# Kernel optimization log

Measured on AMD Instinct MI355X. Metric: run time of the kernel, lower is better.

The kernel has to match this reference:

```python
import jax, jax.numpy as jnp
import numpy as np

B, L, H, E, R = 4, 512, 768, 10, 10

def setup_inputs() -> dict:
    key = jax.random.key(0)
    ks = jax.random.split(key, 7)
    s = 1.0 / np.sqrt(H)
    return {
        "h": jax.random.normal(ks[0], (B, L, H), dtype=jnp.float32),
        "W_proj": jax.random.normal(ks[1], (H, H), dtype=jnp.float32) * s,
        "b_proj": jax.random.normal(ks[2], (H,), dtype=jnp.float32) * s,
        "W_ent": jax.random.normal(ks[3], (E, H), dtype=jnp.float32) * s,
        "b_ent": jax.random.normal(ks[4], (E,), dtype=jnp.float32) * s,
        "W_bil": jax.random.normal(ks[5], (R, H, H), dtype=jnp.float32) * s,
        "b_bil": jax.random.normal(ks[6], (R,), dtype=jnp.float32) * s,
    }

def reference(h, W_proj, b_proj, W_ent, b_ent, W_bil, b_bil):
    # h: (B, L, H)
    h_proj = jax.nn.relu(jnp.einsum('blh,kh->blk', h, W_proj) + b_proj)  # Linear: x @ W^T + b
    ent_logits = jnp.einsum('blh,eh->ble', h_proj, W_ent) + b_ent        # (B, L, E)
    # nn.Bilinear on all (i, j) pairs: rel[b,i,j,r] = h_i^T W_r h_j + b_r.
    # Factored O(L^2*H*R + L*H^2*R) instead of materializing (B,L,L,H) pairs.
    t = jnp.einsum('rhk,bmk->brmh', W_bil, h_proj)                        # (B, R, L, H)
    rel_logits = jnp.einsum('blh,brmh->blmr', h_proj, t) + b_bil          # (B, L, L, R)
    return (ent_logits, rel_logits)
```

## Files before the change

kernel.cpp:

```cpp
#include <hip/hip_runtime.h>
#include <stdint.h>

#define Bdim 4
#define Ldim 512
#define Hdim 768
#define Edim 10
#define Rdim 10

typedef __attribute__((ext_vector_type(8))) short short8;
typedef __attribute__((ext_vector_type(4))) float floatx4;

__device__ __forceinline__ unsigned short f2bf(float x) {
    unsigned int u = __float_as_uint(x);
    unsigned int r = (u + 0x7fffu + ((u >> 16) & 1u)) >> 16;
    return (unsigned short)r;
}
__device__ __forceinline__ float bf2f(unsigned short u) {
    return __uint_as_float(((unsigned int)u) << 16);
}

#define GLOAD_LDS16(g, l)                                                      \
    __builtin_amdgcn_global_load_lds(                                          \
        (const __attribute__((address_space(1))) void*)(g),                    \
        (__attribute__((address_space(3))) void*)(l), 16, 0, 0)

#define WAITVM(n) asm volatile("s_waitcnt vmcnt(" #n ")" ::: "memory")

__device__ __forceinline__ int xcd_swz(int bid, int nwg) {
    int cpx = nwg >> 3;
    return (bid & 7) * cpx + (bid >> 3);
}

__device__ __forceinline__ void gemm_bt_core256_cnt(
    const unsigned short* __restrict__ A, int lda,
    const unsigned short* __restrict__ Bm, int ldb,
    unsigned short* lA, unsigned short* lB,
    floatx4 acc[8][4])
{
    const int tid  = threadIdx.x;
    const int lane = tid & 63;
    const int wave = tid >> 6;
    const int wr = wave >> 2;
    const int wc = wave & 3;

    const int srow   = tid >> 3;
    const int schunk = (tid & 7) ^ (srow & 7);
    const int skk    = schunk << 3;

    const int frow = lane & 15;
    const int fs   = lane >> 4;

    #define STAGE256(t, buf)                                                   \
        do {                                                                   \
            const int k0s = (t) << 6;                                          \
            unsigned short* dA = lA + (buf) * 16384;                           \
            unsigned short* dB = lB + (buf) * 16384;                           \
            _Pragma("unroll")                                                  \
            for (int i = 0; i < 4; ++i) {                                      \
                GLOAD_LDS16(A  + (size_t)(srow + 64 * i) * lda + k0s + skk,    \
                            dA + (tid + 512 * i) * 8);                         \
                GLOAD_LDS16(Bm + (size_t)(srow + 64 * i) * ldb + k0s + skk,    \
                            dB + (tid + 512 * i) * 8);                         \
            }                                                                  \
        } while (0)

    #define COMPUTE256(buf)                                                    \
        do {                                                                   \
            const unsigned short* sA = lA + (buf) * 16384;                     \
            const unsigned short* sB = lB + (buf) * 16384;                     \
            _Pragma("unroll")                                                  \
            for (int h = 0; h < 2; ++h) {                                      \
                short8 bfr[4];                                                 \
                _Pragma("unroll")                                              \
                for (int ni = 0; ni < 4; ++ni) {                               \
                    int row  = wc * 64 + ni * 16 + frow;                       \
                    int slot = (fs + 4 * h) ^ (row & 7);                       \
                    bfr[ni] = *reinterpret_cast<const short8*>(                \
                        sB + row * 64 + slot * 8);                             \
                }                                                              \
                _Pragma("unroll")                                              \
                for (int mi = 0; mi < 8; ++mi) {                               \
                    int row  = wr * 128 + mi * 16 + frow;                      \
                    int slot = (fs + 4 * h) ^ (row & 7);                       \
                    short8 af = *reinterpret_cast<const short8*>(              \
                        sA + row * 64 + slot * 8);                             \
                    _Pragma("unroll")                                          \
                    for (int ni = 0; ni < 4; ++ni)                             \
                        acc[mi][ni] = __builtin_amdgcn_mfma_f32_16x16x32_bf16( \
                            af, bfr[ni], acc[mi][ni], 0, 0, 0);                \
                }                                                              \
            }                                                                  \
        } while (0)

    const int NT = Hdim >> 6;

    STAGE256(0, 0);
    for (int kt = 0; kt < NT - 1; ++kt) {
        __builtin_amdgcn_s_barrier();
        STAGE256(kt + 1, (kt + 1) & 1);
        WAITVM(8);
        __builtin_amdgcn_s_barrier();
        __builtin_amdgcn_sched_barrier(0);
        COMPUTE256(kt & 1);
    }
    __builtin_amdgcn_s_barrier();
    WAITVM(0);
    __builtin_amdgcn_s_barrier();
    __builtin_amdgcn_sched_barrier(0);
    COMPUTE256((NT - 1) & 1);

    #undef STAGE256
    #undef COMPUTE256
}

__global__ __launch_bounds__(256) void k_prep(
    const float* __restrict__ h,   const float* __restrict__ Wp,
    const float* __restrict__ bproj,
    const float* __restrict__ Wbil, const float* __restrict__ We,
    unsigned short* __restrict__ hp,
    unsigned short* __restrict__ Wb_bf, unsigned short* __restrict__ We_bf)
{
    __shared__ unsigned short lA[128 * 64];
    __shared__ unsigned short lB[128 * 64];
    const int tid = threadIdx.x;

    if (blockIdx.x >= 96) {
        const int n2 = Rdim * Hdim * Hdim / 4;
        const int n3 = Edim * Hdim / 4;
        int i = (blockIdx.x - 96) * 256 + tid;
        const int stride = (gridDim.x - 96) * 256;
        for (; i < n2 + n3; i += stride) {
            const float* s; unsigned short* d; int j = i;
            if (j < n2) { s = Wbil; d = Wb_bf; }
            else { j -= n2; s = We; d = We_bf; }
            float4 v = reinterpret_cast<const float4*>(s)[j];
            ushort4 o;
            o.x = f2bf(v.x); o.y = f2bf(v.y); o.z = f2bf(v.z); o.w = f2bf(v.w);
            reinterpret_cast<ushort4*>(d)[j] = o;
        }
        return;
    }

    int bid = xcd_swz(blockIdx.x, 96);
    const int m0 = (bid % 16) * 128;
    const int n0 = (bid / 16) * 128;
    const float* Asrc = h  + (size_t)m0 * Hdim;
    const float* Bsrc = Wp + (size_t)n0 * Hdim;

    const int lane = tid & 63;
    const int wave = tid >> 6;
    const int wr = wave >> 1, wc = wave & 1;
    const int frow = lane & 15;
    const int fs   = lane >> 4;

    floatx4 acc[4][4];
    #pragma unroll
    for (int i = 0; i < 4; ++i)
        #pragma unroll
        for (int j = 0; j < 4; ++j)
            acc[i][j] = (floatx4){0.f, 0.f, 0.f, 0.f};

    float4 ra[4][2], rb[4][2];
    #define LOADREGS(k0s)                                                      \
        _Pragma("unroll")                                                      \
        for (int i = 0; i < 4; ++i) {                                          \
            int q = tid + 256 * i, row = q >> 3, pchk = q & 7;                 \
            int lchk = pchk ^ (row & 7);                                       \
            const float* sa = Asrc + (size_t)row * Hdim + (k0s) + lchk * 8;    \
            const float* sb = Bsrc + (size_t)row * Hdim + (k0s) + lchk * 8;    \
            ra[i][0] = *reinterpret_cast<const float4*>(sa);                   \
            ra[i][1] = *reinterpret_cast<const float4*>(sa + 4);               \
            rb[i][0] = *reinterpret_cast<const float4*>(sb);                   \
            rb[i][1] = *reinterpret_cast<const float4*>(sb + 4);               \
        }

    LOADREGS(0);
    const int NT = Hdim >> 6;
    for (int kt = 0; kt < NT; ++kt) {
        short8 pa[4], pb[4];
        #pragma unroll
        for (int i = 0; i < 4; ++i) {
            pa[i][0] = f2bf(ra[i][0].x); pa[i][1] = f2bf(ra[i][0].y);
            pa[i][2] = f2bf(ra[i][0].z); pa[i][3] = f2bf(ra[i][0].w);
            pa[i][4] = f2bf(ra[i][1].x); pa[i][5] = f2bf(ra[i][1].y);
            pa[i][6] = f2bf(ra[i][1].z); pa[i][7] = f2bf(ra[i][1].w);
            pb[i][0] = f2bf(rb[i][0].x); pb[i][1] = f2bf(rb[i][0].y);
            pb[i][2] = f2bf(rb[i][0].z); pb[i][3] = f2bf(rb[i][0].w);
            pb[i][4] = f2bf(rb[i][1].x); pb[i][5] = f2bf(rb[i][1].y);
            pb[i][6] = f2bf(rb[i][1].z); pb[i][7] = f2bf(rb[i][1].w);
        }
        __syncthreads();
        #pragma unroll
        for (int i = 0; i < 4; ++i) {
            int q = tid + 256 * i, row = q >> 3, pchk = q & 7;
            *reinterpret_cast<short8*>(lA + row * 64 + pchk * 8) = pa[i];
            *reinterpret_cast<short8*>(lB + row * 64 + pchk * 8) = pb[i];
        }
        if (kt + 1 < NT) LOADREGS((kt + 1) << 6);
        __syncthreads();
        #pragma unroll
        for (int hh = 0; hh < 2; ++hh) {
            short8 af[4], bfr[4];
            #pragma unroll
            for (int mi = 0; mi < 4; ++mi) {
                int row  = wr * 64 + mi * 16 + frow;
                int slot = (fs + 4 * hh) ^ (row & 7);
                af[mi] = *reinterpret_cast<const short8*>(lA + row * 64 + slot * 8);
            }
            #pragma unroll
            for (int ni = 0; ni < 4; ++ni) {
                int row  = wc * 64 + ni * 16 + frow;
                int slot = (fs + 4 * hh) ^ (row & 7);
                bfr[ni] = *reinterpret_cast<const short8*>(lB + row * 64 + slot * 8);
            }
            #pragma unroll
            for (int mi = 0; mi < 4; ++mi)
                #pragma unroll
                for (int ni = 0; ni < 4; ++ni)
                    acc[mi][ni] = __builtin_amdgcn_mfma_f32_16x16x32_bf16(
                        af[mi], bfr[ni], acc[mi][ni], 0, 0, 0);
        }
    }
    #undef LOADREGS

    const int cl = lane & 15, rh = (lane >> 4) * 4;
    #pragma unroll
    for (int mi = 0; mi < 4; ++mi)
        #pragma unroll
        for (int ni = 0; ni < 4; ++ni)
            #pragma unroll
            for (int j = 0; j < 4; ++j) {
                int r = m0 + wr * 64 + mi * 16 + rh + j;
                int c = n0 + wc * 64 + ni * 16 + cl;
                float v = acc[mi][ni][j] + bproj[c];
                hp[(size_t)r * Hdim + c] = f2bf(fmaxf(v, 0.0f));
            }
}

__global__ __launch_bounds__(512, 1) void k_gemm_t(
    const unsigned short* __restrict__ hp,
    const unsigned short* __restrict__ Wb,
    unsigned short* __restrict__ T)
{
    __shared__ unsigned short lA[2 * 256 * 64];
    __shared__ unsigned short lB[2 * 256 * 64];
    int bid = xcd_swz(blockIdx.x + gridDim.x * blockIdx.y, gridDim.x * gridDim.y);
    const int m0 = (bid % gridDim.x) * 256;
    const int n0 = (bid / gridDim.x) * 256;
    floatx4 acc[8][4];
    #pragma unroll
    for (int i = 0; i < 8; ++i)
        #pragma unroll
        for (int j = 0; j < 4; ++j)
            acc[i][j] = (floatx4){0.f, 0.f, 0.f, 0.f};

    gemm_bt_core256_cnt(hp + (size_t)m0 * Hdim, Hdim,
                        Wb + (size_t)n0 * Hdim, Hdim, lA, lB, acc);

    const int tid = threadIdx.x, lane = tid & 63, wave = tid >> 6;
    const int wr = wave >> 2, wc = wave & 3;
    const int cl = lane & 15, rh = (lane >> 4) * 4;
    #pragma unroll
    for (int mi = 0; mi < 8; ++mi)
        #pragma unroll
        for (int ni = 0; ni < 4; ++ni)
            #pragma unroll
            for (int j = 0; j < 4; ++j) {
                int r = m0 + wr * 128 + mi * 16 + rh + j;
                int c = n0 + wc * 64 + ni * 16 + cl;
                T[(size_t)r * (Rdim * Hdim) + c] = f2bf(acc[mi][ni][j]);
            }
}

__global__ __launch_bounds__(512, 1) void k_rel_ent(
    const unsigned short* __restrict__ hp,
    const unsigned short* __restrict__ T,
    const float* __restrict__ bbil,
    float* __restrict__ rel,
    const unsigned short* __restrict__ We,
    const float* __restrict__ bent,
    float* __restrict__ out_ent)
{
    __shared__ unsigned short lA[2 * 256 * 64];
    __shared__ unsigned short lB[2 * 256 * 64];
    const int tid = threadIdx.x, lane = tid & 63, wave = tid >> 6;

    if (blockIdx.x >= 160) {
        const int e = blockIdx.x - 160;
        const int base = (e * 8 + wave) * 8;
        for (int rr = 0; rr < 8; ++rr) {
            const unsigned short* row = hp + (size_t)(base + rr) * Hdim;
            float hv[12];
            #pragma unroll
            for (int j = 0; j < 12; ++j) hv[j] = bf2f(row[lane + j * 64]);
            #pragma unroll
            for (int ee = 0; ee < Edim; ++ee) {
                const unsigned short* wrow = We + ee * Hdim;
                float s = 0.f;
                #pragma unroll
                for (int j = 0; j < 12; ++j) s += hv[j] * bf2f(wrow[lane + j * 64]);
                #pragma unroll
                for (int off = 32; off >= 1; off >>= 1) s += __shfl_xor(s, off);
                if (lane == 0) out_ent[(size_t)(base + rr) * Edim + ee] = s + bent[ee];
            }
        }
        return;
    }

    int bid = xcd_swz(blockIdx.x, 160);
    const int m0 = (bid & 7) * 256;
    const int n0 = (bid >> 3) * 256;
    const int b  = m0 >> 9;
    floatx4 acc[8][4];
    #pragma unroll
    for (int i = 0; i < 8; ++i)
        #pragma unroll
        for (int j = 0; j < 4; ++j)
            acc[i][j] = (floatx4){0.f, 0.f, 0.f, 0.f};

    const unsigned short* Ab = hp + (size_t)m0 * Hdim;
    const unsigned short* Bb = T + (size_t)b * Ldim * (Rdim * Hdim) + (size_t)n0 * Hdim;
    gemm_bt_core256_cnt(Ab, Hdim, Bb, Hdim, lA, lB, acc);

    const int wr = wave >> 2, wc = wave & 3;
    const int cl = lane & 15, rh = (lane >> 4) * 4;
    #pragma unroll
    for (int mi = 0; mi < 8; ++mi)
        #pragma unroll
        for (int ni = 0; ni < 4; ++ni) {
            int n = n0 + wc * 64 + ni * 16 + cl;
            float bias = bbil[n % Rdim];
            #pragma unroll
            for (int j = 0; j < 4; ++j) {
                int grow = m0 + wr * 128 + mi * 16 + rh + j;
                rel[(size_t)grow * (Ldim * Rdim) + n] = acc[mi][ni][j] + bias;
            }
        }
}

extern "C" void kernel_launch(void* const* d_in, const int* in_sizes, int n_in,
                              void* d_out, int out_size, void* d_ws, size_t ws_size,
                              hipStream_t stream)
{
    const float* h     = (const float*)d_in[0];
    const float* Wproj = (const float*)d_in[1];
    const float* bproj = (const float*)d_in[2];
    const float* Went  = (const float*)d_in[3];
    const float* bent  = (const float*)d_in[4];
    const float* Wbil  = (const float*)d_in[5];
    const float* bbil  = (const float*)d_in[6];

    float* out_ent = (float*)d_out;
    float* out_rel = (float*)d_out + (size_t)Bdim * Ldim * Edim;

    unsigned short* Wb_bf = (unsigned short*)d_ws;
    unsigned short* We_bf = Wb_bf + (size_t)Rdim * Hdim * Hdim;
    unsigned short* hp_bf = We_bf + (size_t)Edim * Hdim;
    unsigned short* T_bf  = hp_bf + (size_t)2048 * Hdim;

    k_prep<<<dim3(1120), 256, 0, stream>>>(h, Wproj, bproj, Wbil, Went,
                                           hp_bf, Wb_bf, We_bf);

    k_gemm_t<<<dim3(2048 / 256, (Rdim * Hdim) / 256), 512, 0, stream>>>(hp_bf, Wb_bf, T_bf);

    k_rel_ent<<<dim3(192), 512, 0, stream>>>(hp_bf, T_bf, bbil, out_rel,
                                             We_bf, bent, out_ent);
}
```

Before: 169.4 us.

## Retile relation GEMM to 256x160 tiles and move entity head into T-GEMM launch

The entity-logit blocks move from the relation kernel into the T-projection GEMM launch, which now runs 240 GEMM tiles plus 32 entity blocks in one grid. The relation GEMM gets its own kernel with 256x160 output tiles, giving 256 blocks instead of 160 so all CUs are covered. It has a custom double-buffered LDS pipeline and a 4x2 wave layout where each wave computes 64x80. This trades the tuned 256x256 core for a narrower tile with lower per-block reuse and more hand-written loading code, in exchange for better load balance across the GPU.

```diff
diff --git a/kernel.cpp b/kernel.cpp
--- a/kernel.cpp
+++ b/kernel.cpp
@@ -237,46 +237,10 @@
             }
 }
 
-__global__ __launch_bounds__(512, 1) void k_gemm_t(
+__global__ __launch_bounds__(512, 1) void k_gemm_t_ent(
     const unsigned short* __restrict__ hp,
     const unsigned short* __restrict__ Wb,
-    unsigned short* __restrict__ T)
-{
-    __shared__ unsigned short lA[2 * 256 * 64];
-    __shared__ unsigned short lB[2 * 256 * 64];
-    int bid = xcd_swz(blockIdx.x + gridDim.x * blockIdx.y, gridDim.x * gridDim.y);
-    const int m0 = (bid % gridDim.x) * 256;
-    const int n0 = (bid / gridDim.x) * 256;
-    floatx4 acc[8][4];
-    #pragma unroll
-    for (int i = 0; i < 8; ++i)
-        #pragma unroll
-        for (int j = 0; j < 4; ++j)
-            acc[i][j] = (floatx4){0.f, 0.f, 0.f, 0.f};
-
-    gemm_bt_core256_cnt(hp + (size_t)m0 * Hdim, Hdim,
-                        Wb + (size_t)n0 * Hdim, Hdim, lA, lB, acc);
-
-    const int tid = threadIdx.x, lane = tid & 63, wave = tid >> 6;
-    const int wr = wave >> 2, wc = wave & 3;
-    const int cl = lane & 15, rh = (lane >> 4) * 4;
-    #pragma unroll
-    for (int mi = 0; mi < 8; ++mi)
-        #pragma unroll
-        for (int ni = 0; ni < 4; ++ni)
-            #pragma unroll
-            for (int j = 0; j < 4; ++j) {
-                int r = m0 + wr * 128 + mi * 16 + rh + j;
-                int c = n0 + wc * 64 + ni * 16 + cl;
-                T[(size_t)r * (Rdim * Hdim) + c] = f2bf(acc[mi][ni][j]);
-            }
-}
-
-__global__ __launch_bounds__(512, 1) void k_rel_ent(
-    const unsigned short* __restrict__ hp,
-    const unsigned short* __restrict__ T,
-    const float* __restrict__ bbil,
-    float* __restrict__ rel,
+    unsigned short* __restrict__ T,
     const unsigned short* __restrict__ We,
     const float* __restrict__ bent,
     float* __restrict__ out_ent)
@@ -285,9 +249,8 @@
     __shared__ unsigned short lB[2 * 256 * 64];
     const int tid = threadIdx.x, lane = tid & 63, wave = tid >> 6;
 
-    if (blockIdx.x >= 160) {
-        const int e = blockIdx.x - 160;
-        const int base = (e * 8 + wave) * 8;
+    if (blockIdx.x >= 240) {
+        const int base = ((blockIdx.x - 240) * 8 + wave) * 8;
         for (int rr = 0; rr < 8; ++rr) {
             const unsigned short* row = hp + (size_t)(base + rr) * Hdim;
             float hv[12];
@@ -307,10 +270,9 @@
         return;
     }
 
-    int bid = xcd_swz(blockIdx.x, 160);
-    const int m0 = (bid & 7) * 256;
-    const int n0 = (bid >> 3) * 256;
-    const int b  = m0 >> 9;
+    int bid = xcd_swz(blockIdx.x, 240);
+    const int m0 = (bid % 8) * 256;
+    const int n0 = (bid / 8) * 256;
     floatx4 acc[8][4];
     #pragma unroll
     for (int i = 0; i < 8; ++i)
@@ -318,21 +280,131 @@
         for (int j = 0; j < 4; ++j)
             acc[i][j] = (floatx4){0.f, 0.f, 0.f, 0.f};
 
-    const unsigned short* Ab = hp + (size_t)m0 * Hdim;
-    const unsigned short* Bb = T + (size_t)b * Ldim * (Rdim * Hdim) + (size_t)n0 * Hdim;
-    gemm_bt_core256_cnt(Ab, Hdim, Bb, Hdim, lA, lB, acc);
+    gemm_bt_core256_cnt(hp + (size_t)m0 * Hdim, Hdim,
+                        Wb + (size_t)n0 * Hdim, Hdim, lA, lB, acc);
 
     const int wr = wave >> 2, wc = wave & 3;
     const int cl = lane & 15, rh = (lane >> 4) * 4;
     #pragma unroll
     for (int mi = 0; mi < 8; ++mi)
         #pragma unroll
-        for (int ni = 0; ni < 4; ++ni) {
-            int n = n0 + wc * 64 + ni * 16 + cl;
+        for (int ni = 0; ni < 4; ++ni)
+            #pragma unroll
+            for (int j = 0; j < 4; ++j) {
+                int r = m0 + wr * 128 + mi * 16 + rh + j;
+                int c = n0 + wc * 64 + ni * 16 + cl;
+                T[(size_t)r * (Rdim * Hdim) + c] = f2bf(acc[mi][ni][j]);
+            }
+}
+
+__global__ __launch_bounds__(512, 1) void k_rel(
+    const unsigned short* __restrict__ hp,
+    const unsigned short* __restrict__ T,
+    const float* __restrict__ bbil,
+    float* __restrict__ rel)
+{
+    __shared__ unsigned short lA[2 * 256 * 64];
+    __shared__ unsigned short lB[2 * 192 * 64];
+    const int tid = threadIdx.x, lane = tid & 63, wave = tid >> 6;
+    const int wr = wave >> 1;
+    const int wv = wave & 1;
+
+    int bid = xcd_swz(blockIdx.x, 256);
+    const int m0 = (bid & 7) * 256;
+    const int n0 = (bid >> 3) * 160;
+    const int b  = m0 >> 9;
+
+    const unsigned short* A  = hp + (size_t)m0 * Hdim;
+    const unsigned short* Bm = T + (size_t)b * Ldim * (Rdim * Hdim) + (size_t)n0 * Hdim;
+
+    const int srow   = tid >> 3;
+    const int schunk = (tid & 7) ^ (srow & 7);
+    const int skk    = schunk << 3;
+    const int brow2  = (srow >= 32) ? (srow + 64) : (srow + 128);
+
+    const int frow = lane & 15;
+    const int fs   = lane >> 4;
+
+    floatx4 acc[4][5];
+    #pragma unroll
+    for (int i = 0; i < 4; ++i)
+        #pragma unroll
+        for (int j = 0; j < 5; ++j)
+            acc[i][j] = (floatx4){0.f, 0.f, 0.f, 0.f};
+
+    #define STAGE_R(t, buf)                                                    \
+        do {                                                                   \
+            const int k0s = (t) << 6;                                          \
+            unsigned short* dA = lA + (buf) * 16384;                           \
+            unsigned short* dB = lB + (buf) * 12288;                           \
+            _Pragma("unroll")                                                  \
+            for (int i = 0; i < 4; ++i)                                        \
+                GLOAD_LDS16(A + (size_t)(srow + 64 * i) * Hdim + k0s + skk,    \
+                            dA + (tid + 512 * i) * 8);                         \
+            GLOAD_LDS16(Bm + (size_t)srow * Hdim + k0s + skk,                  \
+                        dB + tid * 8);                                         \
+            GLOAD_LDS16(Bm + (size_t)(srow + 64) * Hdim + k0s + skk,           \
+                        dB + (tid + 512) * 8);                                 \
+            GLOAD_LDS16(Bm + (size_t)brow2 * Hdim + k0s + skk,                 \
+                        dB + (tid + 1024) * 8);                                \
+        } while (0)
+
+    #define COMPUTE_R(buf)                                                     \
+        do {                                                                   \
+            const unsigned short* sA = lA + (buf) * 16384;                     \
+            const unsigned short* sB = lB + (buf) * 12288;                     \
+            _Pragma("unroll")                                                  \
+            for (int h = 0; h < 2; ++h) {                                      \
+                short8 bfr[5];                                                 \
+                _Pragma("unroll")                                              \
+                for (int ni = 0; ni < 5; ++ni) {                               \
+                    int row  = wv * 80 + ni * 16 + frow;                       \
+                    int slot = (fs + 4 * h) ^ (row & 7);                       \
+                    bfr[ni] = *reinterpret_cast<const short8*>(                \
+                        sB + row * 64 + slot * 8);                             \
+                }                                                              \
+                _Pragma("unroll")                                              \
+                for (int mi = 0; mi < 4; ++mi) {                               \
+                    int row  = wr * 64 + mi * 16 + frow;                       \
+                    int slot = (fs + 4 * h) ^ (row & 7);                       \
+                    short8 af = *reinterpret_cast<const short8*>(              \
+                        sA + row * 64 + slot * 8);                             \
+                    _Pragma("unroll")                                          \
+                    for (int ni = 0; ni < 5; ++ni)                             \
+                        acc[mi][ni] = __builtin_amdgcn_mfma_f32_16x16x32_bf16( \
+                            af, bfr[ni], acc[mi][ni], 0, 0, 0);                \
+                }                                                              \
+            }                                                                  \
+        } while (0)
+
+    const int NT = Hdim >> 6;
+    STAGE_R(0, 0);
+    for (int kt = 0; kt < NT - 1; ++kt) {
+        __builtin_amdgcn_s_barrier();
+        STAGE_R(kt + 1, (kt + 1) & 1);
+        WAITVM(7);
+        __builtin_amdgcn_s_barrier();
+        __builtin_amdgcn_sched_barrier(0);
+        COMPUTE_R(kt & 1);
+    }
+    __builtin_amdgcn_s_barrier();
+    WAITVM(0);
+    __builtin_amdgcn_s_barrier();
+    __builtin_amdgcn_sched_barrier(0);
+    COMPUTE_R((NT - 1) & 1);
+    #undef STAGE_R
+    #undef COMPUTE_R
+
+    const int cl = lane & 15, rh = (lane >> 4) * 4;
+    #pragma unroll
+    for (int mi = 0; mi < 4; ++mi)
+        #pragma unroll
+        for (int ni = 0; ni < 5; ++ni) {
+            int n = n0 + wv * 80 + ni * 16 + cl;
             float bias = bbil[n % Rdim];
             #pragma unroll
             for (int j = 0; j < 4; ++j) {
-                int grow = m0 + wr * 128 + mi * 16 + rh + j;
+                int grow = m0 + wr * 64 + mi * 16 + rh + j;
                 rel[(size_t)grow * (Ldim * Rdim) + n] = acc[mi][ni][j] + bias;
             }
         }
@@ -361,8 +433,8 @@
     k_prep<<<dim3(1120), 256, 0, stream>>>(h, Wproj, bproj, Wbil, Went,
                                            hp_bf, Wb_bf, We_bf);
 
-    k_gemm_t<<<dim3(2048 / 256, (Rdim * Hdim) / 256), 512, 0, stream>>>(hp_bf, Wb_bf, T_bf);
-
-    k_rel_ent<<<dim3(192), 512, 0, stream>>>(hp_bf, T_bf, bbil, out_rel,
-                                             We_bf, bent, out_ent);
-}
+    k_gemm_t_ent<<<dim3(272), 512, 0, stream>>>(hp_bf, Wb_bf, T_bf,
+                                                We_bf, bent, out_ent);
+
+    k_rel<<<dim3(256), 512, 0, stream>>>(hp_bf, T_bf, bbil, out_rel);
+}
```

After: 187.0 us. 1.1x slower.

## Switch GEMMs to 128x128 single-buffered tiles and move entity head into T kernel

Applied to the files above, without the earlier changes.

Replaces the 256x256, 512-thread double-buffered GEMM core with a 128x128, 256-thread single-buffered core running several blocks per CU. The smaller tiles produce more workgroups (960 for T, 640 for rel) to fill the CUs better, and occupancy replaces the explicit prefetch pipeline as the latency hiding. The entity-logit computation moves from the rel kernel into the T-GEMM kernel. The trade-off is lower per-tile data reuse and no explicit overlap of loads with MFMA.

```diff
diff --git a/kernel.cpp b/kernel.cpp
--- a/kernel.cpp
+++ b/kernel.cpp
@@ -24,93 +24,60 @@
         (const __attribute__((address_space(1))) void*)(g),                    \
         (__attribute__((address_space(3))) void*)(l), 16, 0, 0)
 
-#define WAITVM(n) asm volatile("s_waitcnt vmcnt(" #n ")" ::: "memory")
-
 __device__ __forceinline__ int xcd_swz(int bid, int nwg) {
     int cpx = nwg >> 3;
     return (bid & 7) * cpx + (bid >> 3);
 }
 
-__device__ __forceinline__ void gemm_bt_core256_cnt(
+__device__ __forceinline__ void gemm_bt_core128_sb(
     const unsigned short* __restrict__ A, int lda,
     const unsigned short* __restrict__ Bm, int ldb,
     unsigned short* lA, unsigned short* lB,
-    floatx4 acc[8][4])
+    floatx4 acc[4][4])
 {
     const int tid  = threadIdx.x;
     const int lane = tid & 63;
     const int wave = tid >> 6;
-    const int wr = wave >> 2;
-    const int wc = wave & 3;
-
-    const int srow   = tid >> 3;
-    const int schunk = (tid & 7) ^ (srow & 7);
-    const int skk    = schunk << 3;
-
+    const int wr = wave >> 1;
+    const int wc = wave & 1;
     const int frow = lane & 15;
     const int fs   = lane >> 4;
 
-    #define STAGE256(t, buf)                                                   \
-        do {                                                                   \
-            const int k0s = (t) << 6;                                          \
-            unsigned short* dA = lA + (buf) * 16384;                           \
-            unsigned short* dB = lB + (buf) * 16384;                           \
-            _Pragma("unroll")                                                  \
-            for (int i = 0; i < 4; ++i) {                                      \
-                GLOAD_LDS16(A  + (size_t)(srow + 64 * i) * lda + k0s + skk,    \
-                            dA + (tid + 512 * i) * 8);                         \
-                GLOAD_LDS16(Bm + (size_t)(srow + 64 * i) * ldb + k0s + skk,    \
-                            dB + (tid + 512 * i) * 8);                         \
-            }                                                                  \
-        } while (0)
-
-    #define COMPUTE256(buf)                                                    \
-        do {                                                                   \
-            const unsigned short* sA = lA + (buf) * 16384;                     \
-            const unsigned short* sB = lB + (buf) * 16384;                     \
-            _Pragma("unroll")                                                  \
-            for (int h = 0; h < 2; ++h) {                                      \
-                short8 bfr[4];                                                 \
-                _Pragma("unroll")                                              \
-                for (int ni = 0; ni < 4; ++ni) {                               \
-                    int row  = wc * 64 + ni * 16 + frow;                       \
-                    int slot = (fs + 4 * h) ^ (row & 7);                       \
-                    bfr[ni] = *reinterpret_cast<const short8*>(                \
-                        sB + row * 64 + slot * 8);                             \
-                }                                                              \
-                _Pragma("unroll")                                              \
-                for (int mi = 0; mi < 8; ++mi) {                               \
-                    int row  = wr * 128 + mi * 16 + frow;                      \
-                    int slot = (fs + 4 * h) ^ (row & 7);                       \
-                    short8 af = *reinterpret_cast<const short8*>(              \
-                        sA + row * 64 + slot * 8);                             \
-                    _Pragma("unroll")                                          \
-                    for (int ni = 0; ni < 4; ++ni)                             \
-                        acc[mi][ni] = __builtin_amdgcn_mfma_f32_16x16x32_bf16( \
-                            af, bfr[ni], acc[mi][ni], 0, 0, 0);                \
-                }                                                              \
-            }                                                                  \
-        } while (0)
-
     const int NT = Hdim >> 6;
-
-    STAGE256(0, 0);
-    for (int kt = 0; kt < NT - 1; ++kt) {
-        __builtin_amdgcn_s_barrier();
-        STAGE256(kt + 1, (kt + 1) & 1);
-        WAITVM(8);
-        __builtin_amdgcn_s_barrier();
-        __builtin_amdgcn_sched_barrier(0);
-        COMPUTE256(kt & 1);
+    for (int kt = 0; kt < NT; ++kt) {
+        const int k0 = kt << 6;
+        if (kt) __builtin_amdgcn_s_barrier();
+        #pragma unroll
+        for (int i = 0; i < 4; ++i) {
+            int q = tid + 256 * i, row = q >> 3, pchk = q & 7;
+            int lchk = pchk ^ (row & 7);
+            GLOAD_LDS16(A  + (size_t)row * lda + k0 + lchk * 8, lA + q * 8);
+            GLOAD_LDS16(Bm + (size_t)row * ldb + k0 + lchk * 8, lB + q * 8);
+        }
+        __syncthreads();
+        #pragma unroll
+        for (int h = 0; h < 2; ++h) {
+            short8 af[4], bfr[4];
+            #pragma unroll
+            for (int mi = 0; mi < 4; ++mi) {
+                int row  = wr * 64 + mi * 16 + frow;
+                int slot = (fs + 4 * h) ^ (row & 7);
+                af[mi] = *reinterpret_cast<const short8*>(lA + row * 64 + slot * 8);
+            }
+            #pragma unroll
+            for (int ni = 0; ni < 4; ++ni) {
+                int row  = wc * 64 + ni * 16 + frow;
+                int slot = (fs + 4 * h) ^ (row & 7);
+                bfr[ni] = *reinterpret_cast<const short8*>(lB + row * 64 + slot * 8);
+            }
+            #pragma unroll
+            for (int mi = 0; mi < 4; ++mi)
+                #pragma unroll
+                for (int ni = 0; ni < 4; ++ni)
+                    acc[mi][ni] = __builtin_amdgcn_mfma_f32_16x16x32_bf16(
+                        af[mi], bfr[ni], acc[mi][ni], 0, 0, 0);
+        }
     }
-    __builtin_amdgcn_s_barrier();
-    WAITVM(0);
-    __builtin_amdgcn_s_barrier();
-    __builtin_amdgcn_sched_barrier(0);
-    COMPUTE256((NT - 1) & 1);
-
-    #undef STAGE256
-    #undef COMPUTE256
 }
 
 __global__ __launch_bounds__(256) void k_prep(
@@ -237,58 +204,21 @@
             }
 }
 
-__global__ __launch_bounds__(512, 1) void k_gemm_t(
+__global__ __launch_bounds__(256, 4) void k_gemm_t_ent(
     const unsigned short* __restrict__ hp,
     const unsigned short* __restrict__ Wb,
-    unsigned short* __restrict__ T)
-{
-    __shared__ unsigned short lA[2 * 256 * 64];
-    __shared__ unsigned short lB[2 * 256 * 64];
-    int bid = xcd_swz(blockIdx.x + gridDim.x * blockIdx.y, gridDim.x * gridDim.y);
-    const int m0 = (bid % gridDim.x) * 256;
-    const int n0 = (bid / gridDim.x) * 256;
-    floatx4 acc[8][4];
-    #pragma unroll
-    for (int i = 0; i < 8; ++i)
-        #pragma unroll
-        for (int j = 0; j < 4; ++j)
-            acc[i][j] = (floatx4){0.f, 0.f, 0.f, 0.f};
-
-    gemm_bt_core256_cnt(hp + (size_t)m0 * Hdim, Hdim,
-                        Wb + (size_t)n0 * Hdim, Hdim, lA, lB, acc);
-
-    const int tid = threadIdx.x, lane = tid & 63, wave = tid >> 6;
-    const int wr = wave >> 2, wc = wave & 3;
-    const int cl = lane & 15, rh = (lane >> 4) * 4;
-    #pragma unroll
-    for (int mi = 0; mi < 8; ++mi)
-        #pragma unroll
-        for (int ni = 0; ni < 4; ++ni)
-            #pragma unroll
-            for (int j = 0; j < 4; ++j) {
-                int r = m0 + wr * 128 + mi * 16 + rh + j;
-                int c = n0 + wc * 64 + ni * 16 + cl;
-                T[(size_t)r * (Rdim * Hdim) + c] = f2bf(acc[mi][ni][j]);
-            }
-}
-
-__global__ __launch_bounds__(512, 1) void k_rel_ent(
-    const unsigned short* __restrict__ hp,
-    const unsigned short* __restrict__ T,
-    const float* __restrict__ bbil,
-    float* __restrict__ rel,
+    unsigned short* __restrict__ T,
     const unsigned short* __restrict__ We,
     const float* __restrict__ bent,
     float* __restrict__ out_ent)
 {
-    __shared__ unsigned short lA[2 * 256 * 64];
-    __shared__ unsigned short lB[2 * 256 * 64];
+    __shared__ unsigned short lA[128 * 64];
+    __shared__ unsigned short lB[128 * 64];
     const int tid = threadIdx.x, lane = tid & 63, wave = tid >> 6;
 
-    if (blockIdx.x >= 160) {
-        const int e = blockIdx.x - 160;
-        const int base = (e * 8 + wave) * 8;
-        for (int rr = 0; rr < 8; ++rr) {
+    if (blockIdx.x < 16) {
+        const int base = (blockIdx.x * 4 + wave) * 32;
+        for (int rr = 0; rr < 32; ++rr) {
             const unsigned short* row = hp + (size_t)(base + rr) * Hdim;
             float hv[12];
             #pragma unroll
@@ -307,32 +237,69 @@
         return;
     }
 
-    int bid = xcd_swz(blockIdx.x, 160);
-    const int m0 = (bid & 7) * 256;
-    const int n0 = (bid >> 3) * 256;
-    const int b  = m0 >> 9;
-    floatx4 acc[8][4];
-    #pragma unroll
-    for (int i = 0; i < 8; ++i)
+    int bid = xcd_swz(blockIdx.x - 16, 960);
+    const int m0 = (bid % 16) * 128;
+    const int n0 = (bid / 16) * 128;
+    floatx4 acc[4][4];
+    #pragma unroll
+    for (int i = 0; i < 4; ++i)
         #pragma unroll
         for (int j = 0; j < 4; ++j)
             acc[i][j] = (floatx4){0.f, 0.f, 0.f, 0.f};
 
+    gemm_bt_core128_sb(hp + (size_t)m0 * Hdim, Hdim,
+                       Wb + (size_t)n0 * Hdim, Hdim, lA, lB, acc);
+
+    const int wr = wave >> 1, wc = wave & 1;
+    const int cl = lane & 15, rh = (lane >> 4) * 4;
+    #pragma unroll
+    for (int mi = 0; mi < 4; ++mi)
+        #pragma unroll
+        for (int ni = 0; ni < 4; ++ni)
+            #pragma unroll
+            for (int j = 0; j < 4; ++j) {
+                int r = m0 + wr * 64 + mi * 16 + rh + j;
+                int c = n0 + wc * 64 + ni * 16 + cl;
+                T[(size_t)r * (Rdim * Hdim) + c] = f2bf(acc[mi][ni][j]);
+            }
+}
+
+__global__ __launch_bounds__(256, 4) void k_rel(
+    const unsigned short* __restrict__ hp,
+    const unsigned short* __restrict__ T,
+    const float* __restrict__ bbil,
+    float* __restrict__ rel)
+{
+    __shared__ unsigned short lA[128 * 64];
+    __shared__ unsigned short lB[128 * 64];
+    const int tid = threadIdx.x, lane = tid & 63, wave = tid >> 6;
+
+    int bid = xcd_swz(blockIdx.x, 640);
+    const int m0 = (bid % 16) * 128;
+    const int n0 = (bid / 16) * 128;
+    const int b  = m0 >> 9;
+    floatx4 acc[4][4];
+    #pragma unroll
+    for (int i = 0; i < 4; ++i)
+        #pragma unroll
+        for (int j = 0; j < 4; ++j)
+            acc[i][j] = (floatx4){0.f, 0.f, 0.f, 0.f};
+
     const unsigned short* Ab = hp + (size_t)m0 * Hdim;
     const unsigned short* Bb = T + (size_t)b * Ldim * (Rdim * Hdim) + (size_t)n0 * Hdim;
-    gemm_bt_core256_cnt(Ab, Hdim, Bb, Hdim, lA, lB, acc);
-
-    const int wr = wave >> 2, wc = wave & 3;
+    gemm_bt_core128_sb(Ab, Hdim, Bb, Hdim, lA, lB, acc);
+
+    const int wr = wave >> 1, wc = wave & 1;
     const int cl = lane & 15, rh = (lane >> 4) * 4;
     #pragma unroll
-    for (int mi = 0; mi < 8; ++mi)
+    for (int mi = 0; mi < 4; ++mi)
         #pragma unroll
         for (int ni = 0; ni < 4; ++ni) {
             int n = n0 + wc * 64 + ni * 16 + cl;
             float bias = bbil[n % Rdim];
             #pragma unroll
             for (int j = 0; j < 4; ++j) {
-                int grow = m0 + wr * 128 + mi * 16 + rh + j;
+                int grow = m0 + wr * 64 + mi * 16 + rh + j;
                 rel[(size_t)grow * (Ldim * Rdim) + n] = acc[mi][ni][j] + bias;
             }
         }
@@ -361,8 +328,8 @@
     k_prep<<<dim3(1120), 256, 0, stream>>>(h, Wproj, bproj, Wbil, Went,
                                            hp_bf, Wb_bf, We_bf);
 
-    k_gemm_t<<<dim3(2048 / 256, (Rdim * Hdim) / 256), 512, 0, stream>>>(hp_bf, Wb_bf, T_bf);
-
-    k_rel_ent<<<dim3(192), 512, 0, stream>>>(hp_bf, T_bf, bbil, out_rel,
-                                             We_bf, bent, out_ent);
-}
+    k_gemm_t_ent<<<dim3(976), 256, 0, stream>>>(hp_bf, Wb_bf, T_bf,
+                                                We_bf, bent, out_ent);
+
+    k_rel<<<dim3(640), 256, 0, stream>>>(hp_bf, T_bf, bbil, out_rel);
+}
```

New measurement: 297.6 us. +75.7%, slower.
